# Performance work log

Hardware: AMD Instinct MI355X
Metric: run time of the kernel (lower is better)

## Reference

```python
import jax, jax.numpy as jnp
import numpy as np

N = 20000        # nodes per type
E = 320000       # edges per type (avg degree 16)
H = 8            # heads
F0 = 128         # initial feature dim
F_UNI = 256      # n_unified
F_OUT = 64       # n_units per layer
N_USER = 20000   # shape_ret[0]
N_CLASSES = 2


def setup_inputs() -> dict:
    key = jax.random.key(0)
    ks = jax.random.split(key, 32)
    nrm = lambda k, s: jax.random.normal(k, s, dtype=jnp.float32) * 0.05
    inp = {
        "hemb0": nrm(ks[0], (N, F0)),
        "hemb1": nrm(ks[1], (N, F0)),
        "W0": nrm(ks[2], (F0, F_UNI)),
        "W1": nrm(ks[3], (F0, F_UNI)),
    }
    i = 4
    for t in range(2):
        for l, fin in enumerate([F_UNI, H * F_OUT]):
            inp[f"g{t}l{l}_w"] = nrm(ks[i], (H, fin, F_OUT)); i += 1
            inp[f"g{t}l{l}_asrc"] = nrm(ks[i], (H, F_OUT)); i += 1
            inp[f"g{t}l{l}_atrg"] = nrm(ks[i], (H, F_OUT)); i += 1
    inp["aw1"] = nrm(ks[i], (F_UNI, F_OUT)); i += 1
    inp["aw2"] = nrm(ks[i], (F_OUT, F_OUT)); i += 1
    inp["am"] = nrm(ks[i], (F_OUT,)); i += 1
    inp["fc_w"] = nrm(ks[i], (F_OUT * 3, N_CLASSES)); i += 1
    inp["fc_b"] = jnp.zeros((N_CLASSES,), jnp.float32); i += 1
    inp["edge0"] = jax.random.randint(ks[i], (2, E), 0, N, dtype=jnp.int32); i += 1
    inp["edge1"] = jax.random.randint(ks[i], (2, E), 0, N, dtype=jnp.int32)
    return inp


def spgat(h, src, trg, w, asrc, atrg):
    """Sparse GAT layer: h [N,f_in], edge list src/trg [E] -> [N,H,f_out]."""
    n = h.shape[0]
    hp = jnp.einsum('nf,hfo->hno', h, w)              # [H,N,O]
    s = jnp.einsum('hno,ho->nh', hp, asrc)            # [N,H]
    t = jnp.einsum('hno,ho->nh', hp, atrg)            # [N,H]
    e = jax.nn.leaky_relu(s[src] + t[trg], negative_slope=0.2)  # [E,H]
    ex = jnp.exp(e - jnp.max(e))                      # global max shift (as in source)
    denom = jax.ops.segment_sum(ex, trg, num_segments=n)[trg] + 1e-16
    alpha = ex / denom                                # [E,H]
    msg = jnp.transpose(hp, (1, 0, 2))[src] * alpha[:, :, None]  # [E,H,O]
    return jax.ops.segment_sum(msg, trg, num_segments=n)         # [N,H,O]


def reference(hemb0, hemb1, W0, W1,
              g0l0_w, g0l0_asrc, g0l0_atrg, g0l1_w, g0l1_asrc, g0l1_atrg,
              g1l0_w, g1l0_asrc, g1l0_atrg, g1l1_w, g1l1_asrc, g1l1_atrg,
              aw1, aw2, am, fc_w, fc_b, edge0, edge1):
    trans0 = hemb0 @ W0                                # [N,F_UNI]
    trans1 = hemb1 @ W1
    stacks = [
        (trans0, edge0, (g0l0_w, g0l0_asrc, g0l0_atrg), (g0l1_w, g0l1_asrc, g0l1_atrg)),
        (trans1, edge1, (g1l0_w, g1l0_asrc, g1l0_atrg), (g1l1_w, g1l1_asrc, g1l1_atrg)),
    ]
    heter = []
    for trans, edge, p0, p1 in stacks:
        src, trg = edge[0], edge[1]
        x = spgat(trans, src, trg, *p0)                # [N,H,F_OUT]
        x = jax.nn.elu(x.reshape(N, -1))               # [N,H*F_OUT]
        x = spgat(x, src, trg, *p1).mean(axis=1)       # [N,F_OUT]
        heter.append(x[:N_USER][:, None, :])
    type_aware = jnp.concatenate(heter, axis=1)        # [N_USER, 2, F_OUT]
    # faithful to source: feature = trans_emb[0] where trans_emb is the LAST
    # type's transformed embedding -> row 0, shape [F_UNI], broadcast over nodes
    feature = trans1[0]
    q = jnp.tanh(feature @ aw1 + type_aware @ aw2)     # [N_USER,2,F_OUT]
    beta = jax.nn.softmax(q @ am, axis=-1)             # [N_USER,2]
    fusion = jnp.einsum('nr,nrd->nd', beta, type_aware)[:, None, :]
    ret = jnp.concatenate([type_aware, fusion], axis=1).reshape(N_USER, -1)
    return jax.nn.log_softmax(ret @ fc_w + fc_b, axis=-1)   # [N_USER, 2]
```

## Files before the change

kernel.cpp:

```cpp
#include <hip/hip_runtime.h>
#include <hip/hip_bf16.h>


typedef __hip_bfloat16 bf16;
typedef __attribute__((ext_vector_type(8))) short short8;
typedef __attribute__((ext_vector_type(4))) float f32x4;

__device__ __forceinline__ float bf2f(bf16 v) { return __bfloat162float(v); }
__device__ __forceinline__ float ldin(const void* p, long i, int f32) {
  return f32 ? ((const float*)p)[i] : bf2f(((const bf16*)p)[i]);
}
__device__ __forceinline__ short f2bfbits(float f) {
  bf16 h = __float2bfloat16(f);
  return *reinterpret_cast<short*>(&h);
}
__device__ __forceinline__ float bfbits2f(short b) {
  unsigned u = ((unsigned)(unsigned short)b) << 16;
  return __uint_as_float(u);
}

struct GArg {
  const void* A[2];
  const void* B[2];
  bf16* C[2];
  const void* sa[2];
  const void* sb[2];
  float* sv[2];
  float* tv[2];
};

struct AArg {
  const bf16* hp[2];
  const float* sv[2];
  const float* tv[2];
  const int* rp[2];
  const int* col[2];
  void* out[2];
};

__global__ __launch_bounds__(64) void detect_kernel(const void* __restrict__ x,
                                                    int* __restrict__ flag) {
  int tid = threadIdx.x;
  float m = 0.f;
  for (int i = tid; i < 2048; i += 64) {
    float v = fabsf(bf2f(((const bf16*)x)[i]));
    if (!(v <= 1e3f)) v = 1e9f;
    m = fmaxf(m, v);
  }
#pragma unroll
  for (int off = 32; off; off >>= 1) m = fmaxf(m, __shfl_xor(m, off));
  if (tid == 0) flag[0] = (m > 1e3f) ? 1 : 0;
}

#define GBM 128
#define GBN 64
#define GBK 64

__device__ __forceinline__ int swz(int row, int kbyte) {
  return row * 128 + (kbyte ^ ((row & 7) << 4));
}

__global__ __launch_bounds__(256) void gemm_mfma(GArg g, int amode, int bmode,
                                                 int M, int K, int Nc,
                                                 const int* __restrict__ flag) {
  __shared__ bf16 As[GBM * GBK];
  __shared__ bf16 Bs[GBN * GBK];
  const int z = blockIdx.z;
  const void* __restrict__ A = g.A[z];
  const void* __restrict__ B = g.B[z];
  bf16* __restrict__ C = g.C[z];
  const void* stasrc = g.sa[z];
  const void* statrg = g.sb[z];
  float* svp = g.sv[z];
  float* tvp = g.tv[z];
  const int f32 = flag[0];
  const int af32 = (amode == 1) ? f32 : 0;
  const int bf32 = (bmode == 2) ? 0 : f32;
  const int m0 = blockIdx.x * GBM;
  const int n0 = blockIdx.y * GBN;
  const int tid = threadIdx.x;
  const int lane = tid & 63;
  const int wrow = (tid >> 6) * 32;

  f32x4 acc[2][4];
#pragma unroll
  for (int m = 0; m < 2; m++)
#pragma unroll
    for (int n = 0; n < 4; n++)
#pragma unroll
      for (int r = 0; r < 4; r++) acc[m][n][r] = 0.f;

  for (int kt = 0; kt < K; kt += GBK) {
#pragma unroll
    for (int j = 0; j < 4; j++) {
      int idx = tid + j * 256;
      int row = idx >> 3;
      int ks = idx & 7;
      int gm = m0 + row;
      short8 v;
#pragma unroll
      for (int e = 0; e < 8; e++) v[e] = 0;
      if (gm < M) {
        long base = (long)gm * K + kt + ks * 8;
        if (!af32) {
          v = *(const short8*)((const bf16*)A + base);
        } else {
          const float* Af = (const float*)A + base;
#pragma unroll
          for (int e = 0; e < 8; e++) v[e] = f2bfbits(Af[e]);
        }
      }
      *(short8*)((char*)As + swz(row, ks * 16)) = v;
    }
    {
      int n = tid & 63;
      int ks0 = tid >> 6;
#pragma unroll
      for (int jj = 0; jj < 2; jj++) {
        int ks = ks0 + jj * 4;
        int k = kt + ks * 8;
        int col = n0 + n;
        long base;
        int cstr;
        if (bmode == 1) { base = ((long)(col >> 6) * K + k) * 64 + (col & 63); cstr = 64; }
        else { base = (long)k * Nc + col; cstr = Nc; }
        short8 v;
        if (bf32) {
          const float* Bf = (const float*)B;
#pragma unroll
          for (int e = 0; e < 8; e++) v[e] = f2bfbits(Bf[base + (long)e * cstr]);
        } else {
          const bf16* Bh = (const bf16*)B;
#pragma unroll
          for (int e = 0; e < 8; e++) v[e] = *(const short*)&Bh[base + (long)e * cstr];
        }
        *(short8*)((char*)Bs + swz(n, ks * 16)) = v;
      }
    }
    __syncthreads();
#pragma unroll
    for (int kh = 0; kh < 2; kh++) {
      int klane = kh * 64 + ((lane >> 4) << 4);
      short8 af[2], bfr[4];
#pragma unroll
      for (int m = 0; m < 2; m++) {
        int row = wrow + m * 16 + (lane & 15);
        af[m] = *(const short8*)((const char*)As + swz(row, klane));
      }
#pragma unroll
      for (int n = 0; n < 4; n++) {
        int col = n * 16 + (lane & 15);
        bfr[n] = *(const short8*)((const char*)Bs + swz(col, klane));
      }
#pragma unroll
      for (int m = 0; m < 2; m++)
#pragma unroll
        for (int n = 0; n < 4; n++)
          acc[m][n] = __builtin_amdgcn_mfma_f32_16x16x32_bf16(af[m], bfr[n], acc[m][n], 0, 0, 0);
    }
    __syncthreads();
  }
  if (svp) {
    const int h = blockIdx.y;
    const int cl = lane & 15;
    float av[4], bv[4];
#pragma unroll
    for (int n = 0; n < 4; n++) {
      av[n] = ldin(stasrc, h * 64 + n * 16 + cl, f32);
      bv[n] = ldin(statrg, h * 64 + n * 16 + cl, f32);
    }
#pragma unroll
    for (int m = 0; m < 2; m++) {
#pragma unroll
      for (int r = 0; r < 4; r++) {
        float s = 0.f, t = 0.f;
#pragma unroll
        for (int n = 0; n < 4; n++) {
          s += acc[m][n][r] * av[n];
          t += acc[m][n][r] * bv[n];
        }
#pragma unroll
        for (int off = 1; off <= 8; off <<= 1) {
          s += __shfl_xor(s, off);
          t += __shfl_xor(t, off);
        }
        int row = m0 + wrow + m * 16 + ((lane >> 4) << 2) + r;
        if (cl == 0 && row < M) {
          svp[(long)row * 8 + h] = s;
          tvp[(long)row * 8 + h] = t;
        }
      }
    }
  }
#pragma unroll
  for (int m = 0; m < 2; m++) {
#pragma unroll
    for (int r = 0; r < 4; r++) {
      int row = m0 + wrow + m * 16 + ((lane >> 4) << 2) + r;
      if (row < M) {
#pragma unroll
        for (int n = 0; n < 4; n++) {
          int col = n0 + n * 16 + (lane & 15);
          C[(long)row * Nc + col] = __float2bfloat16(acc[m][n][r]);
        }
      }
    }
  }
}

__global__ void hist2_kernel(const int* __restrict__ trg0, const int* __restrict__ trg1,
                             int* __restrict__ deg, int E, int N) {
  int e = blockIdx.x * 256 + threadIdx.x;
  if (e < E) atomicAdd(&deg[trg0[e]], 1);
  else if (e < 2 * E) atomicAdd(&deg[N + trg1[e - E]], 1);
}

__global__ __launch_bounds__(1024) void scan_kernel(const int* __restrict__ degb,
                                                    int* __restrict__ rpb,
                                                    int* __restrict__ filb, int N) {
  const int* deg = degb + (long)blockIdx.x * N;
  int* row_ptr = rpb + (long)blockIdx.x * (N + 1);
  int* fil = filb + (long)blockIdx.x * N;
  __shared__ int sums[1024];
  int tid = threadIdx.x;
  int chunk = (N + 1023) >> 10;
  int start = tid * chunk;
  int end = start + chunk;
  if (start > N) start = N;
  if (end > N) end = N;
  int s = 0;
  for (int i = start; i < end; i++) s += deg[i];
  sums[tid] = s;
  __syncthreads();
  for (int off = 1; off < 1024; off <<= 1) {
    int add = (tid >= off) ? sums[tid - off] : 0;
    __syncthreads();
    sums[tid] += add;
    __syncthreads();
  }
  int run = (tid > 0) ? sums[tid - 1] : 0;
  for (int i = start; i < end; i++) {
    row_ptr[i] = run;
    fil[i] = run;
    run += deg[i];
  }
  if (tid == 0) row_ptr[N] = sums[1023];
}

__global__ void fill2_kernel(const int* __restrict__ src0, const int* __restrict__ trg0,
                             const int* __restrict__ src1, const int* __restrict__ trg1,
                             int* __restrict__ filb, int* __restrict__ colb, int E, int N) {
  int e = blockIdx.x * 256 + threadIdx.x;
  if (e < E) {
    int t = trg0[e];
    int pos = atomicAdd(&filb[t], 1);
    colb[pos] = src0[e];
  } else if (e < 2 * E) {
    int ee = e - E;
    int t = trg1[ee];
    int pos = atomicAdd(&filb[N + t], 1);
    colb[E + pos] = src1[ee];
  }
}

__device__ __forceinline__ float exleaky(float v) {
  v = v > 0.f ? v : 0.2f * v;
  return __expf(v);
}

__global__ __launch_bounds__(256) void aggregate(AArg aa, int N, int mode) {
  const int ty = blockIdx.y;
  const bf16* __restrict__ hpb = aa.hp[ty];
  const float* __restrict__ svb = aa.sv[ty];
  const float* __restrict__ tvb = aa.tv[ty];
  const int* __restrict__ rp = aa.rp[ty];
  const int* __restrict__ colv = aa.col[ty];
  void* __restrict__ outp = aa.out[ty];
  const int wid = threadIdx.x >> 6;
  const int lane = threadIdx.x & 63;
  const int n = blockIdx.x * 4 + wid;
  if (n >= N) return;
  const int start = rp[n];
  const int deg = rp[n + 1] - start;
  const int h = lane >> 3;
  const float tvh = tvb[(long)n * 8 + h];
  const bf16* __restrict__ hpc = hpb + lane * 8;

  float acc[8] = {0.f, 0.f, 0.f, 0.f, 0.f, 0.f, 0.f, 0.f};
  float den = 1e-16f;

#define AG_LOAD(EB, V0, V1, V2, V3, Q0, Q1, Q2, Q3)                 \
  {                                                                 \
    int t0 = __shfl(mysrc, (EB) + 0), t1 = __shfl(mysrc, (EB) + 1); \
    int t2 = __shfl(mysrc, (EB) + 2), t3 = __shfl(mysrc, (EB) + 3); \
    V0 = *(const short8*)(hpc + (long)t0 * 512);                    \
    V1 = *(const short8*)(hpc + (long)t1 * 512);                    \
    V2 = *(const short8*)(hpc + (long)t2 * 512);                    \
    V3 = *(const short8*)(hpc + (long)t3 * 512);                    \
    Q0 = svb[(long)t0 * 8 + h];                                     \
    Q1 = svb[(long)t1 * 8 + h];                                     \
    Q2 = svb[(long)t2 * 8 + h];                                     \
    Q3 = svb[(long)t3 * 8 + h];                                     \
  }
#define AG_ACC(V0, V1, V2, V3, Q0, Q1, Q2, Q3)                      \
  {                                                                 \
    float a0 = exleaky(Q0 + tvh), a1 = exleaky(Q1 + tvh);           \
    float a2 = exleaky(Q2 + tvh), a3 = exleaky(Q3 + tvh);           \
    den += a0 + a1 + a2 + a3;                                       \
    _Pragma("unroll")                                               \
    for (int j = 0; j < 8; j++)                                     \
      acc[j] += a0 * bfbits2f(V0[j]) + a1 * bfbits2f(V1[j]) +       \
                a2 * bfbits2f(V2[j]) + a3 * bfbits2f(V3[j]);        \
  }

  for (int base = 0; base < deg; base += 64) {
    int cnt = deg - base;
    if (cnt > 64) cnt = 64;
    int mysrc = (lane < cnt) ? colv[start + base + lane] : 0;
    int nfull = cnt & ~3;
    if (nfull) {
      short8 v0, v1, v2, v3;
      float q0, q1, q2, q3;
      AG_LOAD(0, v0, v1, v2, v3, q0, q1, q2, q3);
      for (int e = 4; e < nfull; e += 4) {
        short8 w0 = v0, w1 = v1, w2 = v2, w3 = v3;
        float p0 = q0, p1 = q1, p2 = q2, p3 = q3;
        AG_LOAD(e, v0, v1, v2, v3, q0, q1, q2, q3);
        AG_ACC(w0, w1, w2, w3, p0, p1, p2, p3);
      }
      AG_ACC(v0, v1, v2, v3, q0, q1, q2, q3);
    }
    for (int e = nfull; e < cnt; e++) {
      int s0 = __shfl(mysrc, e);
      short8 v = *(const short8*)(hpc + (long)s0 * 512);
      float a = exleaky(svb[(long)s0 * 8 + h] + tvh);
      den += a;
#pragma unroll
      for (int j = 0; j < 8; j++) acc[j] += a * bfbits2f(v[j]);
    }
  }

  const float dinv = 1.f / den;
  if (mode == 0) {
    short8 o8;
#pragma unroll
    for (int j = 0; j < 8; j++) {
      float s = acc[j] * dinv;
      float ev = s > 0.f ? s : expm1f(s);
      o8[j] = f2bfbits(ev);
    }
    *(short8*)((bf16*)outp + (long)n * 512 + lane * 8) = o8;
  } else {
    float r[8];
#pragma unroll
    for (int j = 0; j < 8; j++) r[j] = acc[j] * dinv;
#pragma unroll
    for (int m = 8; m <= 32; m <<= 1)
#pragma unroll
      for (int j = 0; j < 8; j++) r[j] += __shfl_xor(r[j], m);
    if (lane < 8) {
      float* o = (float*)outp + (long)n * 128 + lane * 8;
#pragma unroll
      for (int j = 0; j < 8; j++) o[j] = r[j] * 0.125f;
    }
  }
}

__global__ __launch_bounds__(256) void favec2_kernel(const void* __restrict__ hemb1,
                                                     const void* __restrict__ W1,
                                                     const void* __restrict__ aw1,
                                                     float* __restrict__ favec,
                                                     const int* __restrict__ flag) {
  const int f32 = flag[0];
  __shared__ float s_h[128];
  __shared__ float s_r[256];
  __shared__ float part[4][64];
  const int tid = threadIdx.x;
  if (tid < 128) s_h[tid] = ldin(hemb1, tid, f32);
  __syncthreads();
  float r = 0.f;
  for (int i = 0; i < 128; i++) r += s_h[i] * ldin(W1, (long)i * 256 + tid, f32);
  s_r[tid] = r;
  __syncthreads();
  const int o = tid & 63;
  const int wv = tid >> 6;
  float acc = 0.f;
#pragma unroll
  for (int kk = 0; kk < 64; kk++) {
    int k = wv * 64 + kk;
    acc += s_r[k] * ldin(aw1, (long)k * 64 + o, f32);
  }
  part[wv][o] = acc;
  __syncthreads();
  if (tid < 64) favec[o] = part[0][o] + part[1][o] + part[2][o] + part[3][o];
}

#define FN 16
__global__ __launch_bounds__(256) void final_kernel(const float* __restrict__ ta,
                                                    const float* __restrict__ favec,
                                                    const void* __restrict__ aw2,
                                                    const void* __restrict__ am,
                                                    const void* __restrict__ fcw,
                                                    const void* __restrict__ fcb,
                                                    void* __restrict__ out, int N,
                                                    const int* __restrict__ flag) {
  const int f32 = flag[0];
  __shared__ float s_w[64 * 64];
  __shared__ float s_fc[384];
  __shared__ float s_misc[130];
  __shared__ float s_ta[FN * 128];
  const int tid = threadIdx.x;
  const int n0 = blockIdx.x * FN;
  for (int i = tid; i < 4096; i += 256) s_w[i] = ldin(aw2, i, f32);
  for (int i = tid; i < 384; i += 256) s_fc[i] = ldin(fcw, i, f32);
  if (tid < 64) s_misc[tid] = favec[tid];
  else if (tid < 128) s_misc[tid] = ldin(am, tid - 64, f32);
  else if (tid < 130) s_misc[tid] = ldin(fcb, tid - 128, f32);
  for (int idx = tid; idx < FN * 128; idx += 256) {
    int ni = idx >> 7;
    int j = idx & 127;
    int k = j >> 1, r = j & 1;
    int n = n0 + ni;
    s_ta[idx] = (n < N) ? ta[(long)n * 128 + r * 64 + k] : 0.f;
  }
  __syncthreads();
  const int o = tid & 63;
  const int wv = tid >> 6;
#pragma unroll
  for (int ni4 = 0; ni4 < 4; ni4++) {
    const int ni = wv * 4 + ni4;
    const int n = n0 + ni;
    if (n >= N) continue;
    const float* tb = &s_ta[ni * 128];
    float acc0 = s_misc[o], acc1 = acc0;
#pragma unroll 8
    for (int k = 0; k < 64; k++) {
      float2 t2 = *(const float2*)(tb + k * 2);
      float w = s_w[k * 64 + o];
      acc0 += t2.x * w;
      acc1 += t2.y * w;
    }
    float ta0 = tb[o * 2];
    float ta1 = tb[o * 2 + 1];
    float amv = s_misc[64 + o];
    float p0 = tanhf(acc0) * amv;
    float p1 = tanhf(acc1) * amv;
#pragma unroll
    for (int off = 32; off > 0; off >>= 1) {
      p0 += __shfl_xor(p0, off);
      p1 += __shfl_xor(p1, off);
    }
    float mx = fmaxf(p0, p1);
    float e0 = __expf(p0 - mx), e1 = __expf(p1 - mx);
    float b0 = e0 / (e0 + e1), b1 = e1 / (e0 + e1);
    float fus = b0 * ta0 + b1 * ta1;
    float l0 = ta0 * s_fc[o * 2 + 0] + ta1 * s_fc[(64 + o) * 2 + 0] + fus * s_fc[(128 + o) * 2 + 0];
    float l1 = ta0 * s_fc[o * 2 + 1] + ta1 * s_fc[(64 + o) * 2 + 1] + fus * s_fc[(128 + o) * 2 + 1];
#pragma unroll
    for (int off = 32; off > 0; off >>= 1) {
      l0 += __shfl_xor(l0, off);
      l1 += __shfl_xor(l1, off);
    }
    if (o == 0) {
      l0 += s_misc[128];
      l1 += s_misc[129];
      float m2 = fmaxf(l0, l1);
      float lse = m2 + logf(__expf(l0 - m2) + __expf(l1 - m2));
      if (f32) {
        ((float*)out)[n * 2 + 0] = l0 - lse;
        ((float*)out)[n * 2 + 1] = l1 - lse;
      } else {
        ((bf16*)out)[n * 2 + 0] = __float2bfloat16(l0 - lse);
        ((bf16*)out)[n * 2 + 1] = __float2bfloat16(l1 - lse);
      }
    }
  }
}

extern "C" void kernel_launch(void* const* d_in, const int* in_sizes, int n_in,
                              void* d_out, int out_size, void* d_ws, size_t ws_size,
                              hipStream_t stream) {
  constexpr int N = 20000, E = 320000, H = 8, F0 = 128, FU = 256, FO = 64;
  const void* hemb[2] = {d_in[0], d_in[1]};
  const void* W[2] = {d_in[2], d_in[3]};
  const void* gw[2][2] = {{d_in[4], d_in[7]}, {d_in[10], d_in[13]}};
  const void* gasrc[2][2] = {{d_in[5], d_in[8]}, {d_in[11], d_in[14]}};
  const void* gatrg[2][2] = {{d_in[6], d_in[9]}, {d_in[12], d_in[15]}};
  const void* aw1 = d_in[16];
  const void* aw2 = d_in[17];
  const void* am = d_in[18];
  const void* fcw = d_in[19];
  const void* fcb = d_in[20];
  const int* edge[2] = {(const int*)d_in[21], (const int*)d_in[22]};

  const size_t szWg = (size_t)F0 * 512 * 2;
  const size_t szHp = (size_t)N * 512 * 2;
  const size_t szSv = (size_t)N * 8 * 4;
  size_t need = 0;
  auto addsz = [&](size_t b) { need += (b + 255) & ~(size_t)255; };
  addsz(4);
  addsz(szWg * 2);
  addsz(szHp * 2); addsz(szHp * 2);
  addsz(szSv * 2); addsz(szSv * 2);
  addsz((size_t)N * 128 * 4); addsz(256);
  addsz((size_t)2 * N * 4); addsz((size_t)2 * (N + 1) * 4);
  addsz((size_t)2 * N * 4); addsz((size_t)2 * E * 4);
  const bool batched = (ws_size >= need + 4096);
  const int TB = batched ? 2 : 1;

  char* p = (char*)d_ws;
  auto alloc = [&](size_t bytes) -> void* {
    void* r = (void*)p;
    p += (bytes + 255) & ~(size_t)255;
    return r;
  };
  int* flag = (int*)alloc(4);
  bf16* wg = (bf16*)alloc(szWg * 2);
  bf16* hp = (bf16*)alloc(szHp * TB);
  bf16* xbuf = (bf16*)alloc(szHp * TB);
  float* sv = (float*)alloc(szSv * TB);
  float* tv = (float*)alloc(szSv * TB);
  float* ta = (float*)alloc((size_t)N * 128 * 4);
  float* favec = (float*)alloc(256);
  int* degb = (int*)alloc((size_t)2 * N * 4);
  int* rpb = (int*)alloc((size_t)2 * (N + 1) * 4);
  int* filb = (int*)alloc((size_t)2 * N * 4);
  int* colb = (int*)alloc((size_t)2 * E * 4);

  detect_kernel<<<1, 64, 0, stream>>>(hemb[0], flag);

  hipMemsetAsync(degb, 0, (size_t)2 * N * 4, stream);
  hist2_kernel<<<(2 * E + 255) / 256, 256, 0, stream>>>(edge[0] + E, edge[1] + E, degb, E, N);
  scan_kernel<<<2, 1024, 0, stream>>>(degb, rpb, filb, N);
  fill2_kernel<<<(2 * E + 255) / 256, 256, 0, stream>>>(edge[0], edge[0] + E,
                                                        edge[1], edge[1] + E, filb, colb, E, N);

  favec2_kernel<<<1, 256, 0, stream>>>(hemb[1], W[1], aw1, favec, flag);

  {
    GArg gW{};
    for (int i = 0; i < 2; i++) {
      gW.A[i] = W[i]; gW.B[i] = gw[i][0]; gW.C[i] = wg + (size_t)i * F0 * 512;
      gW.sa[i] = nullptr; gW.sb[i] = nullptr; gW.sv[i] = nullptr; gW.tv[i] = nullptr;
    }
    gemm_mfma<<<dim3(1, (H * FO) / GBN, 2), 256, 0, stream>>>(gW, 1, 1, F0, FU, H * FO, flag);
  }

  const int gmx = (N + GBM - 1) / GBM;
  const int npass = batched ? 1 : 2;
  const int TC = batched ? 2 : 1;

  auto hpP = [&](int b) { return hp + (size_t)b * N * 512; };
  auto xbufP = [&](int b) { return xbuf + (size_t)b * N * 512; };
  auto svP = [&](int b) { return sv + (size_t)b * N * 8; };
  auto tvP = [&](int b) { return tv + (size_t)b * N * 8; };

  for (int pass = 0; pass < npass; pass++) {
    int types[2] = {batched ? 0 : pass, batched ? 1 : pass};
    int bufs[2] = {0, batched ? 1 : 0};

    GArg g1{};
    for (int i = 0; i < TC; i++) {
      int t = types[i], b = bufs[i];
      g1.A[i] = hemb[t]; g1.B[i] = wg + (size_t)t * F0 * 512; g1.C[i] = hpP(b);
      g1.sa[i] = gasrc[t][0]; g1.sb[i] = gatrg[t][0]; g1.sv[i] = svP(b); g1.tv[i] = tvP(b);
    }
    gemm_mfma<<<dim3(gmx, (H * FO) / GBN, TC), 256, 0, stream>>>(g1, 1, 2, N, F0, H * FO, flag);

    AArg a0{};
    for (int i = 0; i < TC; i++) {
      int t = types[i], b = bufs[i];
      a0.hp[i] = hpP(b); a0.sv[i] = svP(b); a0.tv[i] = tvP(b);
      a0.rp[i] = rpb + (size_t)t * (N + 1); a0.col[i] = colb + (size_t)t * E;
      a0.out[i] = xbufP(b);
    }
    aggregate<<<dim3((N + 3) / 4, TC), 256, 0, stream>>>(a0, N, 0);

    GArg g2{};
    for (int i = 0; i < TC; i++) {
      int t = types[i], b = bufs[i];
      g2.A[i] = xbufP(b); g2.B[i] = gw[t][1]; g2.C[i] = hpP(b);
      g2.sa[i] = gasrc[t][1]; g2.sb[i] = gatrg[t][1]; g2.sv[i] = svP(b); g2.tv[i] = tvP(b);
    }
    gemm_mfma<<<dim3(gmx, (H * FO) / GBN, TC), 256, 0, stream>>>(g2, 0, 1, N, H * FO, H * FO, flag);

    AArg a1{};
    for (int i = 0; i < TC; i++) {
      int t = types[i], b = bufs[i];
      a1.hp[i] = hpP(b); a1.sv[i] = svP(b); a1.tv[i] = tvP(b);
      a1.rp[i] = rpb + (size_t)t * (N + 1); a1.col[i] = colb + (size_t)t * E;
      a1.out[i] = ta + (size_t)t * FO;
    }
    aggregate<<<dim3((N + 3) / 4, TC), 256, 0, stream>>>(a1, N, 1);
  }

  final_kernel<<<(N + FN - 1) / FN, 256, 0, stream>>>(ta, favec, aw2, am, fcw, fcb, d_out, N, flag);
}
```

Baseline: 569.9 us.

## Add full-K GEMM for first GAT projection and vectorize tile loads

```diff
diff --git a/kernel.cpp b/kernel.cpp
--- a/kernel.cpp
+++ b/kernel.cpp
@@ -106,36 +106,39 @@
           v = *(const short8*)((const bf16*)A + base);
         } else {
           const float* Af = (const float*)A + base;
-#pragma unroll
-          for (int e = 0; e < 8; e++) v[e] = f2bfbits(Af[e]);
+          float4 x0 = *(const float4*)Af;
+          float4 x1 = *(const float4*)(Af + 4);
+          v[0] = f2bfbits(x0.x); v[1] = f2bfbits(x0.y);
+          v[2] = f2bfbits(x0.z); v[3] = f2bfbits(x0.w);
+          v[4] = f2bfbits(x1.x); v[5] = f2bfbits(x1.y);
+          v[6] = f2bfbits(x1.z); v[7] = f2bfbits(x1.w);
         }
       }
       *(short8*)((char*)As + swz(row, ks * 16)) = v;
     }
-    {
-      int n = tid & 63;
-      int ks0 = tid >> 6;
-#pragma unroll
-      for (int jj = 0; jj < 2; jj++) {
-        int ks = ks0 + jj * 4;
-        int k = kt + ks * 8;
-        int col = n0 + n;
-        long base;
-        int cstr;
-        if (bmode == 1) { base = ((long)(col >> 6) * K + k) * 64 + (col & 63); cstr = 64; }
-        else { base = (long)k * Nc + col; cstr = Nc; }
-        short8 v;
-        if (bf32) {
-          const float* Bf = (const float*)B;
-#pragma unroll
-          for (int e = 0; e < 8; e++) v[e] = f2bfbits(Bf[base + (long)e * cstr]);
-        } else {
-          const bf16* Bh = (const bf16*)B;
-#pragma unroll
-          for (int e = 0; e < 8; e++) v[e] = *(const short*)&Bh[base + (long)e * cstr];
-        }
-        *(short8*)((char*)Bs + swz(n, ks * 16)) = v;
-      }
+#pragma unroll
+    for (int j = 0; j < 2; j++) {
+      int idx = tid + j * 256;
+      int k = idx >> 3;
+      int colblk = idx & 7;
+      long base;
+      if (bmode == 1) base = ((long)blockIdx.y * K + kt + k) * 64 + colblk * 8;
+      else base = (long)(kt + k) * Nc + n0 + colblk * 8;
+      short8 v;
+      if (bf32) {
+        const float* Bf = (const float*)B + base;
+        float4 x0 = *(const float4*)Bf;
+        float4 x1 = *(const float4*)(Bf + 4);
+        v[0] = f2bfbits(x0.x); v[1] = f2bfbits(x0.y);
+        v[2] = f2bfbits(x0.z); v[3] = f2bfbits(x0.w);
+        v[4] = f2bfbits(x1.x); v[5] = f2bfbits(x1.y);
+        v[6] = f2bfbits(x1.z); v[7] = f2bfbits(x1.w);
+      } else {
+        v = *(const short8*)((const bf16*)B + base);
+      }
+#pragma unroll
+      for (int e = 0; e < 8; e++)
+        *(short*)((char*)Bs + swz(colblk * 8 + e, k * 2)) = v[e];
     }
     __syncthreads();
 #pragma unroll
@@ -205,6 +208,128 @@
         }
       }
     }
+  }
+}
+
+#define FKBM 64
+
+__device__ __forceinline__ int swz256(int row, int kbyte) {
+  return row * 256 + (kbyte ^ ((row & 7) << 4));
+}
+
+__global__ __launch_bounds__(256) void gemm_fullk(GArg g, int M,
+                                                  const int* __restrict__ flag) {
+  __shared__ bf16 As[FKBM * 128];
+  __shared__ bf16 Bs[64 * 128];
+  const int z = blockIdx.z;
+  const void* __restrict__ A = g.A[z];
+  const bf16* __restrict__ B = (const bf16*)g.B[z];
+  bf16* __restrict__ C = g.C[z];
+  const void* stasrc = g.sa[z];
+  const void* statrg = g.sb[z];
+  float* svp = g.sv[z];
+  float* tvp = g.tv[z];
+  const int f32 = flag[0];
+  const int m0 = blockIdx.x * FKBM;
+  const int tid = threadIdx.x;
+  const int lane = tid & 63;
+  const int wrow = (tid >> 6) * 16;
+
+#pragma unroll
+  for (int j = 0; j < 4; j++) {
+    int idx = tid + j * 256;
+    int row = idx >> 4;
+    int ks = idx & 15;
+    int gm = m0 + row;
+    short8 v;
+#pragma unroll
+    for (int e = 0; e < 8; e++) v[e] = 0;
+    if (gm < M) {
+      long base = (long)gm * 128 + ks * 8;
+      if (!f32) {
+        v = *(const short8*)((const bf16*)A + base);
+      } else {
+        const float* Af = (const float*)A + base;
+        float4 x0 = *(const float4*)Af;
+        float4 x1 = *(const float4*)(Af + 4);
+        v[0] = f2bfbits(x0.x); v[1] = f2bfbits(x0.y);
+        v[2] = f2bfbits(x0.z); v[3] = f2bfbits(x0.w);
+        v[4] = f2bfbits(x1.x); v[5] = f2bfbits(x1.y);
+        v[6] = f2bfbits(x1.z); v[7] = f2bfbits(x1.w);
+      }
+    }
+    *(short8*)((char*)As + swz256(row, ks * 16)) = v;
+  }
+
+  for (int p = 0; p < 8; p++) {
+#pragma unroll
+    for (int j = 0; j < 4; j++) {
+      int idx = tid + j * 256;
+      int k = idx >> 3;
+      int colblk = idx & 7;
+      short8 v = *(const short8*)(B + (long)k * 512 + p * 64 + colblk * 8);
+#pragma unroll
+      for (int e = 0; e < 8; e++)
+        *(short*)((char*)Bs + swz256(colblk * 8 + e, k * 2)) = v[e];
+    }
+    __syncthreads();
+    f32x4 acc[4];
+#pragma unroll
+    for (int n = 0; n < 4; n++)
+#pragma unroll
+      for (int r = 0; r < 4; r++) acc[n][r] = 0.f;
+#pragma unroll
+    for (int kb = 0; kb < 4; kb++) {
+      int klane = kb * 64 + ((lane >> 4) << 4);
+      short8 af = *(const short8*)((const char*)As + swz256(wrow + (lane & 15), klane));
+      short8 bfr[4];
+#pragma unroll
+      for (int n = 0; n < 4; n++)
+        bfr[n] = *(const short8*)((const char*)Bs + swz256(n * 16 + (lane & 15), klane));
+#pragma unroll
+      for (int n = 0; n < 4; n++)
+        acc[n] = __builtin_amdgcn_mfma_f32_16x16x32_bf16(af, bfr[n], acc[n], 0, 0, 0);
+    }
+    {
+      const int cl = lane & 15;
+      float av[4], bv[4];
+#pragma unroll
+      for (int n = 0; n < 4; n++) {
+        av[n] = ldin(stasrc, p * 64 + n * 16 + cl, f32);
+        bv[n] = ldin(statrg, p * 64 + n * 16 + cl, f32);
+      }
+#pragma unroll
+      for (int r = 0; r < 4; r++) {
+        float s = 0.f, t = 0.f;
+#pragma unroll
+        for (int n = 0; n < 4; n++) {
+          s += acc[n][r] * av[n];
+          t += acc[n][r] * bv[n];
+        }
+#pragma unroll
+        for (int off = 1; off <= 8; off <<= 1) {
+          s += __shfl_xor(s, off);
+          t += __shfl_xor(t, off);
+        }
+        int row = m0 + wrow + ((lane >> 4) << 2) + r;
+        if (cl == 0 && row < M) {
+          svp[(long)row * 8 + p] = s;
+          tvp[(long)row * 8 + p] = t;
+        }
+      }
+    }
+#pragma unroll
+    for (int r = 0; r < 4; r++) {
+      int row = m0 + wrow + ((lane >> 4) << 2) + r;
+      if (row < M) {
+#pragma unroll
+        for (int n = 0; n < 4; n++) {
+          int col = p * 64 + n * 16 + (lane & 15);
+          C[(long)row * 512 + col] = __float2bfloat16(acc[n][r]);
+        }
+      }
+    }
+    __syncthreads();
   }
 }
 
@@ -547,6 +672,7 @@
   }
 
   const int gmx = (N + GBM - 1) / GBM;
+  const int gfk = (N + FKBM - 1) / FKBM;
   const int npass = batched ? 1 : 2;
   const int TC = batched ? 2 : 1;
 
@@ -565,7 +691,7 @@
       g1.A[i] = hemb[t]; g1.B[i] = wg + (size_t)t * F0 * 512; g1.C[i] = hpP(b);
       g1.sa[i] = gasrc[t][0]; g1.sb[i] = gatrg[t][0]; g1.sv[i] = svP(b); g1.tv[i] = tvP(b);
     }
-    gemm_mfma<<<dim3(gmx, (H * FO) / GBN, TC), 256, 0, stream>>>(g1, 1, 2, N, F0, H * FO, flag);
+    gemm_fullk<<<dim3(gfk, 1, TC), 256, 0, stream>>>(g1, N, flag);
 
     AArg a0{};
     for (int i = 0; i < TC; i++) {
```

Result: no change. 575.6 us (+1.0%).
